# Performance work log

Hardware: AMD Instinct MI355X
Metric: run time of the kernel (lower is better)

## Reference

```python
import jax, jax.numpy as jnp
import numpy as np

D_MODEL = 1024
D_INNER = 2048
N_EXPERTS = 8
TOP_K = 2
INIT_STD = 0.02


def setup_inputs() -> dict:
    key = jax.random.key(0)
    ks = jax.random.split(key, 6)
    B, S = 2, 2048
    x = jax.random.normal(ks[0], (B, S, D_MODEL), dtype=jnp.float32)
    router_w = jax.random.normal(ks[1], (N_EXPERTS, D_MODEL), dtype=jnp.float32) * (INIT_STD * 0.1)
    router_b = jnp.zeros((N_EXPERTS,), dtype=jnp.float32)
    gate_w = jax.random.normal(ks[2], (N_EXPERTS, D_MODEL, D_INNER), dtype=jnp.float32) * INIT_STD
    up_w = jax.random.normal(ks[3], (N_EXPERTS, D_MODEL, D_INNER), dtype=jnp.float32) * INIT_STD
    down_w = jax.random.normal(ks[4], (N_EXPERTS, D_INNER, D_MODEL), dtype=jnp.float32) * INIT_STD
    return {"x": x, "router_w": router_w, "router_b": router_b,
            "gate_w": gate_w, "up_w": up_w, "down_w": down_w}


def reference(x, router_w, router_b, gate_w, up_w, down_w):
    # Router: softmax over experts, top-k, renormalize top-k probs.
    logits = jnp.einsum('bsd,ed->bse', x, router_w) + router_b          # [B,S,E]
    probs = jax.nn.softmax(logits, axis=-1)
    top_p, top_i = jax.lax.top_k(probs, TOP_K)                           # [B,S,K]
    top_p = top_p / jnp.sum(top_p, axis=-1, keepdims=True)
    # Per-expert combine weight: c[b,s,e] = sum_k top_p[b,s,k] * [top_i[b,s,k]==e]
    onehot = jax.nn.one_hot(top_i, N_EXPERTS, dtype=x.dtype)             # [B,S,K,E]
    combine = jnp.einsum('bsk,bske->bse', top_p, onehot)                 # [B,S,E]
    # SwiGLU FFN for every expert (dense form of the masked dispatch),
    # zeroed/weighted by combine coefficients.
    g = jnp.einsum('bsd,edf->ebsf', x, gate_w)                           # [E,B,S,F]
    u = jnp.einsum('bsd,edf->ebsf', x, up_w)
    h = jax.nn.silu(g) * u
    y = jnp.einsum('ebsf,efd->ebsd', h, down_w)                          # [E,B,S,D]
    out = jnp.einsum('ebsd,bse->bsd', y, combine)
    return out
```

## Files before the change

kernel.cpp:

```cpp
#include <hip/hip_runtime.h>
#include <hip/hip_bf16.h>
#include <stdint.h>

#define D_MODEL 1024
#define D_INNER 2048
#define NEXP 8
#define TOPK 2
#define T256 40
#define T128 72

typedef float f32x4 __attribute__((ext_vector_type(4)));
typedef short bf16x8 __attribute__((ext_vector_type(8)));

#define MEMFENCE asm volatile("" ::: "memory")
#define SB __builtin_amdgcn_sched_barrier(0)
#define LGKM0 asm volatile("s_waitcnt lgkmcnt(0)" ::: "memory")
#define VM0 asm volatile("s_waitcnt vmcnt(0)" ::: "memory")
#define VM4 asm volatile("s_waitcnt vmcnt(4)" ::: "memory")
#define BAR __builtin_amdgcn_s_barrier()
#define SW2(r) (((r) >> 1) & 3)

__device__ __forceinline__ unsigned short f2b(float f) {
    union { float f; uint32_t u; } v; v.f = f;
    uint32_t u = v.u;
    return (unsigned short)((u + 0x7fffu + ((u >> 16) & 1u)) >> 16);
}

__device__ __forceinline__ void gl_lds16(const void* g, void* l) {
    __builtin_amdgcn_global_load_lds((const __attribute__((address_space(1))) void*)g,
                                     (__attribute__((address_space(3))) void*)l, 16, 0, 0);
}

__global__ __launch_bounds__(256) void tcast3_kernel(
    const float* __restrict__ gw, const float* __restrict__ uw, const float* __restrict__ dw,
    unsigned short* __restrict__ gT, unsigned short* __restrict__ uT, unsigned short* __restrict__ dT)
{
    __shared__ unsigned short S[64][68];
    int which = blockIdx.z >> 3;
    int e = blockIdx.z & 7;
    const float* in; unsigned short* out; int K, N;
    if (which == 0)      { in = gw; out = gT; K = D_MODEL; N = D_INNER; }
    else if (which == 1) { in = uw; out = uT; K = D_MODEL; N = D_INNER; }
    else                 { in = dw; out = dT; K = D_INNER; N = D_MODEL; }
    int n0 = blockIdx.x * 64, k0 = blockIdx.y * 64;
    if (n0 >= N || k0 >= K) return;
    const float* ib = in + (size_t)e * K * N;
    unsigned short* ob = out + (size_t)e * N * K;
    int tid = threadIdx.x;
    int kk = tid >> 4, nn4 = (tid & 15) * 4;
#pragma unroll
    for (int j = 0; j < 4; j++) {
        int k = kk + 16 * j;
        float4 v = *(const float4*)&ib[(size_t)(k0 + k) * N + n0 + nn4];
        ushort4 s; s.x = f2b(v.x); s.y = f2b(v.y); s.z = f2b(v.z); s.w = f2b(v.w);
        *(ushort4*)&S[k][nn4] = s;
    }
    __syncthreads();
    int nn = tid >> 4, kk4 = (tid & 15) * 4;
#pragma unroll
    for (int j = 0; j < 4; j++) {
        int n = nn + 16 * j;
        ushort4 s;
        s.x = S[kk4 + 0][n]; s.y = S[kk4 + 1][n];
        s.z = S[kk4 + 2][n]; s.w = S[kk4 + 3][n];
        *(ushort4*)&ob[(size_t)(n0 + n) * K + k0 + kk4] = s;
    }
}

__global__ __launch_bounds__(64) void router_kernel(
    const float* __restrict__ x, const float* __restrict__ rw,
    const float* __restrict__ rb, unsigned short* __restrict__ xb,
    int* __restrict__ top_i, float* __restrict__ top_w, int T)
{
    int t = blockIdx.x;
    if (t >= T) return;
    int l = threadIdx.x;
    float xv[16];
#pragma unroll
    for (int i = 0; i < 16; i++) xv[i] = x[(size_t)t * D_MODEL + l + 64 * i];
#pragma unroll
    for (int i = 0; i < 16; i++) xb[(size_t)t * D_MODEL + l + 64 * i] = f2b(xv[i]);
    float logit[NEXP];
#pragma unroll
    for (int e = 0; e < NEXP; e++) {
        float acc = 0.f;
#pragma unroll
        for (int i = 0; i < 16; i++) acc += xv[i] * rw[e * D_MODEL + l + 64 * i];
#pragma unroll
        for (int s = 32; s > 0; s >>= 1) acc += __shfl_xor(acc, s, 64);
        logit[e] = acc + rb[e];
    }
    if (l == 0) {
        int i0 = 0; float m0 = logit[0];
#pragma unroll
        for (int e = 1; e < NEXP; e++) if (logit[e] > m0) { m0 = logit[e]; i0 = e; }
        int i1 = -1; float m1 = -3.0e38f;
#pragma unroll
        for (int e = 0; e < NEXP; e++) {
            if (e == i0) continue;
            if (logit[e] > m1) { m1 = logit[e]; i1 = e; }
        }
        float w0 = 1.f / (1.f + expf(m1 - m0));
        top_i[t * 2 + 0] = i0; top_i[t * 2 + 1] = i1;
        top_w[t * 2 + 0] = w0; top_w[t * 2 + 1] = 1.f - w0;
    }
}

__global__ __launch_bounds__(256) void bucket_kernel(
    const int* __restrict__ top_i, const float* __restrict__ top_w,
    int* __restrict__ meta, int* __restrict__ tok_of_slot,
    float* __restrict__ w_of_slot, int T)
{
    __shared__ int cnt[256][NEXP];
    __shared__ int pre[256][NEXP];
    __shared__ int tot[NEXP];
    __shared__ int off[NEXP + 1];
    int tid = threadIdx.x;
    int per = (T + 255) / 256;
    int t0 = tid * per;
    for (int e = 0; e < NEXP; e++) cnt[tid][e] = 0;
    for (int t = t0; t < t0 + per && t < T; t++)
        for (int k = 0; k < TOPK; k++) cnt[tid][top_i[t * 2 + k]]++;
    __syncthreads();
    if (tid < NEXP) {
        int run = 0;
        for (int i = 0; i < 256; i++) { pre[i][tid] = run; run += cnt[i][tid]; }
        tot[tid] = run;
    }
    __syncthreads();
    if (tid == 0) {
        off[0] = 0;
        for (int e = 0; e < NEXP; e++) off[e + 1] = off[e] + tot[e];
        for (int e = 0; e <= NEXP; e++) meta[e] = off[e];
        int nt = 0;
        for (int e = 0; e < NEXP; e++)
            for (int r = off[e]; r < off[e + 1]; r += 256)
                meta[16 + nt++] = (e << 16) | r;
        meta[11] = nt;
        for (; nt < T256; nt++) meta[16 + nt] = -1;
        nt = 0;
        for (int e = 0; e < NEXP; e++)
            for (int r = off[e]; r < off[e + 1]; r += 128)
                meta[64 + nt++] = (e << 16) | r;
        meta[12] = nt;
        for (; nt < T128; nt++) meta[64 + nt] = -1;
    }
    __syncthreads();
    int lc[NEXP];
#pragma unroll
    for (int e = 0; e < NEXP; e++) lc[e] = 0;
    for (int t = t0; t < t0 + per && t < T; t++) {
        for (int k = 0; k < TOPK; k++) {
            int e = top_i[t * 2 + k];
            int slot = off[e] + pre[tid][e] + lc[e]++;
            tok_of_slot[slot] = t;
            w_of_slot[slot] = top_w[t * 2 + k];
        }
    }
}

__global__ __launch_bounds__(256, 3) void moe_gate_up(
    const unsigned short* __restrict__ xb, const unsigned short* __restrict__ wgT,
    const unsigned short* __restrict__ wuT, const int* __restrict__ meta,
    const int* __restrict__ tok_of_slot, unsigned short* __restrict__ H)
{
    extern __shared__ __align__(16) unsigned short lds[];

    int lin = blockIdx.x;
    int strip = (lin & 7) * 4 + ((lin >> 3) & 3);
    int tix = lin >> 5;
    int packed = meta[64 + tix];
    if (packed < 0) return;
    int e = packed >> 16, row0 = packed & 0xffff;
    int Mloc = min(128, meta[e + 1] - row0);
    int f0 = strip * 64;

    int tid = threadIdx.x, wv = tid >> 6, lane = tid & 63;
    int lrow = lane & 15, kgrp = lane >> 4;
    int sel = wv & 1, wm = wv >> 1;
    int co = 8 * (kgrp ^ SW2(lrow));

    const unsigned short* sA[2];
    int dA[2];
#pragma unroll
    for (int j = 0; j < 2; j++) {
        int idx = j * 256 + tid;
        int r = idx >> 2, c = idx & 3;
        int slot = row0 + ((r < Mloc) ? r : 0);
        sA[j] = xb + (size_t)tok_of_slot[slot] * D_MODEL + 8 * (c ^ SW2(r));
        dA[j] = idx * 8;
    }
    const unsigned short *sG, *sU;
    {
        int r = tid >> 2, c = tid & 3;
        size_t wb = (size_t)e * D_MODEL * D_INNER + (size_t)(f0 + r) * D_MODEL + 8 * (c ^ SW2(r));
        sG = wgT + wb; sU = wuT + wb;
    }

    int aoff[4], boff[4];
#pragma unroll
    for (int i = 0; i < 4; i++) aoff[i] = (wm * 64 + i * 16 + lrow) * 32 + co;
    int bb = sel ? 6144 : 4096;
#pragma unroll
    for (int i = 0; i < 4; i++) boff[i] = bb + (i * 16 + lrow) * 32 + co;

    f32x4 acc[4][4];
#pragma unroll
    for (int i = 0; i < 4; i++)
#pragma unroll
        for (int j = 0; j < 4; j++) acc[i][j] = (f32x4){0.f, 0.f, 0.f, 0.f};

    auto stage = [&](int u) {
        int kk = u * 32;
        unsigned short* b = lds + (u % 3) * 8192;
        gl_lds16(sA[0] + kk, b + dA[0]);
        gl_lds16(sA[1] + kk, b + dA[1]);
        gl_lds16(sG + kk, b + 4096 + tid * 8);
        gl_lds16(sU + kk, b + 6144 + tid * 8);
    };

    bf16x8 a[4], bfr[4];
    auto load_frags = [&](int u) {
        const unsigned short* b = lds + (u % 3) * 8192;
#pragma unroll
        for (int i = 0; i < 4; i++) a[i] = *(const bf16x8*)(b + aoff[i]);
#pragma unroll
        for (int i = 0; i < 4; i++) bfr[i] = *(const bf16x8*)(b + boff[i]);
    };

    const int NT = D_MODEL / 32;
    stage(0); stage(1);
    MEMFENCE;
    VM4;
    BAR; MEMFENCE;
    load_frags(0);

    for (int t = 0; t < NT; ++t) {
        if (t + 2 < NT) stage(t + 2);
        SB;
        __builtin_amdgcn_s_setprio(1);
#pragma unroll
        for (int i = 0; i < 4; i++)
#pragma unroll
            for (int j = 0; j < 4; j++)
                acc[i][j] = __builtin_amdgcn_mfma_f32_16x16x32_bf16(a[i], bfr[j], acc[i][j], 0, 0, 0);
        __builtin_amdgcn_s_setprio(0);
        SB;
        LGKM0;
        if (t + 2 < NT) { VM4; } else { VM0; }
        BAR; MEMFENCE;
        if (t + 1 < NT) load_frags(t + 1);
    }

    __syncthreads();
    float* ex = (float*)lds;
    if (sel == 1) {
        float* dst = ex + wm * 4160;
#pragma unroll
        for (int i = 0; i < 4; i++)
#pragma unroll
            for (int j = 0; j < 4; j++)
#pragma unroll
                for (int r = 0; r < 4; r++)
                    dst[(i * 16 + kgrp * 4 + r) * 65 + j * 16 + lrow] = acc[i][j][r];
    }
    __syncthreads();
    if (sel == 0) {
        const float* src = ex + wm * 4160;
#pragma unroll
        for (int i = 0; i < 4; i++)
#pragma unroll
            for (int j = 0; j < 4; j++)
#pragma unroll
                for (int r = 0; r < 4; r++) {
                    int row = i * 16 + kgrp * 4 + r;
                    int m = wm * 64 + row;
                    if (m < Mloc) {
                        float g = acc[i][j][r];
                        float u = src[row * 65 + j * 16 + lrow];
                        float h = g / (1.f + __expf(-g)) * u;
                        H[(size_t)(row0 + m) * D_INNER + f0 + j * 16 + lrow] = f2b(h);
                    }
                }
    }
}

__global__ __launch_bounds__(256, 3) void moe_down(
    const unsigned short* __restrict__ H, const unsigned short* __restrict__ wdT,
    const int* __restrict__ meta, const int* __restrict__ tok_of_slot,
    const float* __restrict__ w_of_slot, float* __restrict__ out, int S2)
{
    extern __shared__ __align__(16) unsigned short lds[];
    __shared__ int toks[128];
    __shared__ float wts[128];

    int lin = blockIdx.x;
    int d0 = (lin & 7) * 128;
    int tix = lin >> 3;
    int packed = meta[64 + tix];
    if (packed < 0) return;
    int e = packed >> 16, row0 = packed & 0xffff;
    int Mloc = min(128, meta[e + 1] - row0);

    int tid = threadIdx.x, wv = tid >> 6, lane = tid & 63;
    int lrow = lane & 15, kgrp = lane >> 4;
    int wn = wv & 1, wm = wv >> 1;
    int co = 8 * (kgrp ^ SW2(lrow));

    if (tid < 128) {
        bool v = tid < Mloc;
        toks[tid] = v ? tok_of_slot[row0 + tid] : 0;
        wts[tid] = v ? w_of_slot[row0 + tid] : 0.f;
    }

    const unsigned short* sA[2];
    const unsigned short* sB[2];
    int dA[2];
#pragma unroll
    for (int j = 0; j < 2; j++) {
        int idx = j * 256 + tid;
        int r = idx >> 2, c = idx & 3;
        int slot = min(row0 + r, S2 - 1);
        sA[j] = H + (size_t)slot * D_INNER + 8 * (c ^ SW2(r));
        sB[j] = wdT + (size_t)e * D_INNER * D_MODEL + (size_t)(d0 + r) * D_INNER + 8 * (c ^ SW2(r));
        dA[j] = idx * 8;
    }

    int aoff[4], boff[4];
#pragma unroll
    for (int i = 0; i < 4; i++) aoff[i] = (wm * 64 + i * 16 + lrow) * 32 + co;
#pragma unroll
    for (int i = 0; i < 4; i++) boff[i] = 4096 + (wn * 64 + i * 16 + lrow) * 32 + co;

    f32x4 acc[4][4];
#pragma unroll
    for (int i = 0; i < 4; i++)
#pragma unroll
        for (int j = 0; j < 4; j++) acc[i][j] = (f32x4){0.f, 0.f, 0.f, 0.f};

    auto stage = [&](int u) {
        int kk = u * 32;
        unsigned short* b = lds + (u % 3) * 8192;
        gl_lds16(sA[0] + kk, b + dA[0]);
        gl_lds16(sA[1] + kk, b + dA[1]);
        gl_lds16(sB[0] + kk, b + 4096 + dA[0]);
        gl_lds16(sB[1] + kk, b + 4096 + dA[1]);
    };

    bf16x8 a[4], bfr[4];
    auto load_frags = [&](int u) {
        const unsigned short* b = lds + (u % 3) * 8192;
#pragma unroll
        for (int i = 0; i < 4; i++) a[i] = *(const bf16x8*)(b + aoff[i]);
#pragma unroll
        for (int i = 0; i < 4; i++) bfr[i] = *(const bf16x8*)(b + boff[i]);
    };

    const int NT = D_INNER / 32;
    stage(0); stage(1);
    MEMFENCE;
    VM4;
    BAR; MEMFENCE;
    load_frags(0);

    for (int t = 0; t < NT; ++t) {
        if (t + 2 < NT) stage(t + 2);
        SB;
        __builtin_amdgcn_s_setprio(1);
#pragma unroll
        for (int i = 0; i < 4; i++)
#pragma unroll
            for (int j = 0; j < 4; j++)
                acc[i][j] = __builtin_amdgcn_mfma_f32_16x16x32_bf16(a[i], bfr[j], acc[i][j], 0, 0, 0);
        __builtin_amdgcn_s_setprio(0);
        SB;
        LGKM0;
        if (t + 2 < NT) { VM4; } else { VM0; }
        BAR; MEMFENCE;
        if (t + 1 < NT) load_frags(t + 1);
    }

#pragma unroll
    for (int i = 0; i < 4; i++)
#pragma unroll
        for (int j = 0; j < 4; j++)
#pragma unroll
            for (int r = 0; r < 4; r++) {
                int m = wm * 64 + i * 16 + kgrp * 4 + r;
                if (m < Mloc) {
                    int n = d0 + wn * 64 + j * 16 + lrow;
                    atomicAdd(&out[(size_t)toks[m] * D_MODEL + n], wts[m] * acc[i][j][r]);
                }
            }
}

extern "C" void kernel_launch(void* const* d_in, const int* in_sizes, int n_in,
                              void* d_out, int out_size, void* d_ws, size_t ws_size,
                              hipStream_t stream) {
    const float* x  = (const float*)d_in[0];
    const float* rw = (const float*)d_in[1];
    const float* rb = (const float*)d_in[2];
    const float* gw = (const float*)d_in[3];
    const float* uw = (const float*)d_in[4];
    const float* dw = (const float*)d_in[5];
    float* out = (float*)d_out;

    int T = in_sizes[0] / D_MODEL;
    int S2 = 2 * T;

    char* ws = (char*)d_ws;
    size_t cur = 0;
    auto take = [&](size_t bytes) { char* p = ws + cur; cur = (cur + bytes + 255) & ~(size_t)255; return p; };
    int*   top_i = (int*)take((size_t)S2 * 4);
    float* top_w = (float*)take((size_t)S2 * 4);
    int*   meta  = (int*)take(1024);
    int*   tos   = (int*)take((size_t)S2 * 4);
    float* wos   = (float*)take((size_t)S2 * 4);
    unsigned short* xb  = (unsigned short*)take((size_t)T * D_MODEL * 2);
    unsigned short* wgT = (unsigned short*)take((size_t)NEXP * D_MODEL * D_INNER * 2);
    unsigned short* wuT = (unsigned short*)take((size_t)NEXP * D_MODEL * D_INNER * 2);
    unsigned short* wdT = (unsigned short*)take((size_t)NEXP * D_MODEL * D_INNER * 2);
    unsigned short* H   = (unsigned short*)take((size_t)S2 * D_INNER * 2);

    static const int RING_LDS = 3 * 8192 * 2;
    hipFuncSetAttribute((const void*)moe_gate_up,
                        hipFuncAttributeMaxDynamicSharedMemorySize, RING_LDS);
    hipFuncSetAttribute((const void*)moe_down,
                        hipFuncAttributeMaxDynamicSharedMemorySize, RING_LDS);

    hipMemsetAsync(d_out, 0, (size_t)out_size * sizeof(float), stream);

    tcast3_kernel<<<dim3(32, 32, 24), 256, 0, stream>>>(gw, uw, dw, wgT, wuT, wdT);
    router_kernel<<<T, 64, 0, stream>>>(x, rw, rb, xb, top_i, top_w, T);
    bucket_kernel<<<1, 256, 0, stream>>>(top_i, top_w, meta, tos, wos, T);

    moe_gate_up<<<T128 * 32, 256, RING_LDS, stream>>>(xb, wgT, wuT, meta, tos, H);
    moe_down<<<T128 * 8, 256, RING_LDS, stream>>>(H, wdT, meta, tos, wos, out, S2);
}
```

Measured before the change: 272.1 us.

## Enlarge MoE GEMM tiles to 512 threads with K=64 stages and split-K down

Both expert GEMMs move to 512-thread blocks with 64-wide K stages in a larger triple-buffered LDS ring, using an XOR swizzle over 8 chunks. Gate/up now covers 256-row token tiles via the T256 tile list, and down uses 256-column tiles with a two-way split-K that accumulates through atomics. Fragment loads and prefetch are interleaved with four MFMA quadrants per stage to overlap LDS reads with compute. The aim is more operand reuse and fewer weight reloads per token. In exchange it adds extra barriers per iteration, raises LDS per block, and doubles atomic traffic in the down projection.

New measurement: 315.4 us. 15.9% more time.

```diff
diff --git a/kernel.cpp b/kernel.cpp
--- a/kernel.cpp
+++ b/kernel.cpp
@@ -16,9 +16,17 @@
 #define SB __builtin_amdgcn_sched_barrier(0)
 #define LGKM0 asm volatile("s_waitcnt lgkmcnt(0)" ::: "memory")
 #define VM0 asm volatile("s_waitcnt vmcnt(0)" ::: "memory")
-#define VM4 asm volatile("s_waitcnt vmcnt(4)" ::: "memory")
+#define VM6 asm volatile("s_waitcnt vmcnt(6)" ::: "memory")
 #define BAR __builtin_amdgcn_s_barrier()
-#define SW2(r) (((r) >> 1) & 3)
+
+#define Q8(I0, J0, AF, BF)                                                        \
+  _Pragma("unroll") for (int i_ = 0; i_ < 2; i_++)                                \
+    _Pragma("unroll") for (int j_ = 0; j_ < 2; j_++) {                            \
+      acc[(I0) + i_][(J0) + j_] = __builtin_amdgcn_mfma_f32_16x16x32_bf16(        \
+          AF[2 * i_], BF[2 * j_], acc[(I0) + i_][(J0) + j_], 0, 0, 0);            \
+      acc[(I0) + i_][(J0) + j_] = __builtin_amdgcn_mfma_f32_16x16x32_bf16(        \
+          AF[2 * i_ + 1], BF[2 * j_ + 1], acc[(I0) + i_][(J0) + j_], 0, 0, 0);    \
+    }
 
 __device__ __forceinline__ unsigned short f2b(float f) {
     union { float f; uint32_t u; } v; v.f = f;
@@ -159,7 +167,7 @@
     }
 }
 
-__global__ __launch_bounds__(256, 3) void moe_gate_up(
+__global__ __launch_bounds__(512, 2) void moe_gate_up(
     const unsigned short* __restrict__ xb, const unsigned short* __restrict__ wgT,
     const unsigned short* __restrict__ wuT, const int* __restrict__ meta,
     const int* __restrict__ tok_of_slot, unsigned short* __restrict__ H)
@@ -169,40 +177,39 @@
     int lin = blockIdx.x;
     int strip = (lin & 7) * 4 + ((lin >> 3) & 3);
     int tix = lin >> 5;
-    int packed = meta[64 + tix];
+    int packed = meta[16 + tix];
     if (packed < 0) return;
     int e = packed >> 16, row0 = packed & 0xffff;
-    int Mloc = min(128, meta[e + 1] - row0);
+    int Mloc = min(256, meta[e + 1] - row0);
     int f0 = strip * 64;
 
     int tid = threadIdx.x, wv = tid >> 6, lane = tid & 63;
-    int lrow = lane & 15, kgrp = lane >> 4;
-    int sel = wv & 1, wm = wv >> 1;
-    int co = 8 * (kgrp ^ SW2(lrow));
-
-    const unsigned short* sA[2];
-    int dA[2];
-#pragma unroll
-    for (int j = 0; j < 2; j++) {
-        int idx = j * 256 + tid;
-        int r = idx >> 2, c = idx & 3;
+    int lrow = lane & 15, kgrp = lane >> 4, sw = lrow & 7;
+    int mh = wv >> 1, sel = wv & 1;
+    int co0 = 8 * (kgrp ^ sw);
+    int co1 = 8 * ((4 + kgrp) ^ sw);
+
+    int srow = tid >> 3, schk = tid & 7;
+    const unsigned short* sA[4];
+#pragma unroll
+    for (int j = 0; j < 4; j++) {
+        int r = j * 64 + srow;
         int slot = row0 + ((r < Mloc) ? r : 0);
-        sA[j] = xb + (size_t)tok_of_slot[slot] * D_MODEL + 8 * (c ^ SW2(r));
-        dA[j] = idx * 8;
+        sA[j] = xb + (size_t)tok_of_slot[slot] * D_MODEL + 8 * (schk ^ (r & 7));
     }
     const unsigned short *sG, *sU;
     {
-        int r = tid >> 2, c = tid & 3;
-        size_t wb = (size_t)e * D_MODEL * D_INNER + (size_t)(f0 + r) * D_MODEL + 8 * (c ^ SW2(r));
+        size_t wb = (size_t)e * D_MODEL * D_INNER + (size_t)(f0 + srow) * D_MODEL + 8 * (schk ^ (srow & 7));
         sG = wgT + wb; sU = wuT + wb;
     }
+    int dst = tid * 8;
 
     int aoff[4], boff[4];
 #pragma unroll
-    for (int i = 0; i < 4; i++) aoff[i] = (wm * 64 + i * 16 + lrow) * 32 + co;
-    int bb = sel ? 6144 : 4096;
-#pragma unroll
-    for (int i = 0; i < 4; i++) boff[i] = bb + (i * 16 + lrow) * 32 + co;
+    for (int i = 0; i < 4; i++) aoff[i] = (mh * 64 + i * 16 + lrow) * 64;
+    int bb = 16384 + sel * 4096;
+#pragma unroll
+    for (int i = 0; i < 4; i++) boff[i] = bb + (i * 16 + lrow) * 64;
 
     f32x4 acc[4][4];
 #pragma unroll
@@ -210,63 +217,81 @@
 #pragma unroll
         for (int j = 0; j < 4; j++) acc[i][j] = (f32x4){0.f, 0.f, 0.f, 0.f};
 
-    auto stage = [&](int u) {
-        int kk = u * 32;
-        unsigned short* b = lds + (u % 3) * 8192;
-        gl_lds16(sA[0] + kk, b + dA[0]);
-        gl_lds16(sA[1] + kk, b + dA[1]);
-        gl_lds16(sG + kk, b + 4096 + tid * 8);
-        gl_lds16(sU + kk, b + 6144 + tid * 8);
-    };
-
-    bf16x8 a[4], bfr[4];
-    auto load_frags = [&](int u) {
-        const unsigned short* b = lds + (u % 3) * 8192;
-#pragma unroll
-        for (int i = 0; i < 4; i++) a[i] = *(const bf16x8*)(b + aoff[i]);
-#pragma unroll
-        for (int i = 0; i < 4; i++) bfr[i] = *(const bf16x8*)(b + boff[i]);
-    };
-
-    const int NT = D_MODEL / 32;
-    stage(0); stage(1);
-    MEMFENCE;
-    VM4;
-    BAR; MEMFENCE;
-    load_frags(0);
+    auto stageA01 = [&](int u) {
+        int kk = u * 64; unsigned short* b = lds + (u % 3) * 24576;
+        gl_lds16(sA[0] + kk, b + dst);
+        gl_lds16(sA[1] + kk, b + 4096 + dst);
+    };
+    auto stageA23 = [&](int u) {
+        int kk = u * 64; unsigned short* b = lds + (u % 3) * 24576;
+        gl_lds16(sA[2] + kk, b + 8192 + dst);
+        gl_lds16(sA[3] + kk, b + 12288 + dst);
+    };
+    auto stageGU = [&](int u) {
+        int kk = u * 64; unsigned short* b = lds + (u % 3) * 24576;
+        gl_lds16(sG + kk, b + 16384 + dst);
+        gl_lds16(sU + kk, b + 20480 + dst);
+    };
+
+    bf16x8 A0[4], A1[4], B0[4], B1[4];
+
+    const int NT = D_MODEL / 64;
+    stageA01(0); stageA23(0); stageGU(0);
+    stageA01(1); stageA23(1); stageGU(1);
+    MEMFENCE; VM6; BAR; MEMFENCE;
 
     for (int t = 0; t < NT; ++t) {
-        if (t + 2 < NT) stage(t + 2);
+        const unsigned short* b = lds + (t % 3) * 24576;
+        bool pf = (t + 2) < NT;
+        A0[0] = *(const bf16x8*)(b + aoff[0] + co0);
+        A0[1] = *(const bf16x8*)(b + aoff[0] + co1);
+        A0[2] = *(const bf16x8*)(b + aoff[1] + co0);
+        A0[3] = *(const bf16x8*)(b + aoff[1] + co1);
+        B0[0] = *(const bf16x8*)(b + boff[0] + co0);
+        B0[1] = *(const bf16x8*)(b + boff[0] + co1);
+        B0[2] = *(const bf16x8*)(b + boff[1] + co0);
+        B0[3] = *(const bf16x8*)(b + boff[1] + co1);
+        if (pf) stageA01(t + 2);
+        SB; BAR; LGKM0; SB;
+        __builtin_amdgcn_s_setprio(1); Q8(0, 0, A0, B0); __builtin_amdgcn_s_setprio(0);
+        SB; BAR;
+        B1[0] = *(const bf16x8*)(b + boff[2] + co0);
+        B1[1] = *(const bf16x8*)(b + boff[2] + co1);
+        B1[2] = *(const bf16x8*)(b + boff[3] + co0);
+        B1[3] = *(const bf16x8*)(b + boff[3] + co1);
+        if (pf) stageA23(t + 2);
+        SB; BAR; LGKM0; SB;
+        __builtin_amdgcn_s_setprio(1); Q8(0, 2, A0, B1); __builtin_amdgcn_s_setprio(0);
+        SB; BAR;
+        A1[0] = *(const bf16x8*)(b + aoff[2] + co0);
+        A1[1] = *(const bf16x8*)(b + aoff[2] + co1);
+        A1[2] = *(const bf16x8*)(b + aoff[3] + co0);
+        A1[3] = *(const bf16x8*)(b + aoff[3] + co1);
+        if (pf) stageGU(t + 2);
+        SB; BAR; LGKM0; SB;
+        __builtin_amdgcn_s_setprio(1); Q8(2, 0, A1, B0); __builtin_amdgcn_s_setprio(0);
+        SB; BAR;
+        __builtin_amdgcn_s_setprio(1); Q8(2, 2, A1, B1); __builtin_amdgcn_s_setprio(0);
         SB;
-        __builtin_amdgcn_s_setprio(1);
-#pragma unroll
-        for (int i = 0; i < 4; i++)
-#pragma unroll
-            for (int j = 0; j < 4; j++)
-                acc[i][j] = __builtin_amdgcn_mfma_f32_16x16x32_bf16(a[i], bfr[j], acc[i][j], 0, 0, 0);
-        __builtin_amdgcn_s_setprio(0);
-        SB;
-        LGKM0;
-        if (t + 2 < NT) { VM4; } else { VM0; }
+        if (pf) { VM6; } else { VM0; }
         BAR; MEMFENCE;
-        if (t + 1 < NT) load_frags(t + 1);
     }
 
     __syncthreads();
     float* ex = (float*)lds;
     if (sel == 1) {
-        float* dst = ex + wm * 4160;
+        float* d = ex + mh * 4160;
 #pragma unroll
         for (int i = 0; i < 4; i++)
 #pragma unroll
             for (int j = 0; j < 4; j++)
 #pragma unroll
                 for (int r = 0; r < 4; r++)
-                    dst[(i * 16 + kgrp * 4 + r) * 65 + j * 16 + lrow] = acc[i][j][r];
+                    d[(i * 16 + kgrp * 4 + r) * 65 + j * 16 + lrow] = acc[i][j][r];
     }
     __syncthreads();
     if (sel == 0) {
-        const float* src = ex + wm * 4160;
+        const float* s = ex + mh * 4160;
 #pragma unroll
         for (int i = 0; i < 4; i++)
 #pragma unroll
@@ -274,10 +299,10 @@
 #pragma unroll
                 for (int r = 0; r < 4; r++) {
                     int row = i * 16 + kgrp * 4 + r;
-                    int m = wm * 64 + row;
+                    int m = mh * 64 + row;
                     if (m < Mloc) {
                         float g = acc[i][j][r];
-                        float u = src[row * 65 + j * 16 + lrow];
+                        float u = s[row * 65 + j * 16 + lrow];
                         float h = g / (1.f + __expf(-g)) * u;
                         H[(size_t)(row0 + m) * D_INNER + f0 + j * 16 + lrow] = f2b(h);
                     }
@@ -285,7 +310,7 @@
     }
 }
 
-__global__ __launch_bounds__(256, 3) void moe_down(
+__global__ __launch_bounds__(512, 2) void moe_down(
     const unsigned short* __restrict__ H, const unsigned short* __restrict__ wdT,
     const int* __restrict__ meta, const int* __restrict__ tok_of_slot,
     const float* __restrict__ w_of_slot, float* __restrict__ out, int S2)
@@ -295,17 +320,21 @@
     __shared__ float wts[128];
 
     int lin = blockIdx.x;
-    int d0 = (lin & 7) * 128;
+    int dstrip = lin & 3;
+    int kq = (lin >> 2) & 1;
     int tix = lin >> 3;
     int packed = meta[64 + tix];
     if (packed < 0) return;
     int e = packed >> 16, row0 = packed & 0xffff;
     int Mloc = min(128, meta[e + 1] - row0);
+    int d0 = dstrip * 256;
+    int kb = kq * 1024;
 
     int tid = threadIdx.x, wv = tid >> 6, lane = tid & 63;
-    int lrow = lane & 15, kgrp = lane >> 4;
-    int wn = wv & 1, wm = wv >> 1;
-    int co = 8 * (kgrp ^ SW2(lrow));
+    int lrow = lane & 15, kgrp = lane >> 4, sw = lrow & 7;
+    int mh = wv >> 2, nh = wv & 3;
+    int co0 = 8 * (kgrp ^ sw);
+    int co1 = 8 * ((4 + kgrp) ^ sw);
 
     if (tid < 128) {
         bool v = tid < Mloc;
@@ -313,24 +342,27 @@
         wts[tid] = v ? w_of_slot[row0 + tid] : 0.f;
     }
 
+    int srow = tid >> 3, schk = tid & 7;
     const unsigned short* sA[2];
-    const unsigned short* sB[2];
-    int dA[2];
 #pragma unroll
     for (int j = 0; j < 2; j++) {
-        int idx = j * 256 + tid;
-        int r = idx >> 2, c = idx & 3;
+        int r = j * 64 + srow;
         int slot = min(row0 + r, S2 - 1);
-        sA[j] = H + (size_t)slot * D_INNER + 8 * (c ^ SW2(r));
-        sB[j] = wdT + (size_t)e * D_INNER * D_MODEL + (size_t)(d0 + r) * D_INNER + 8 * (c ^ SW2(r));
-        dA[j] = idx * 8;
-    }
+        sA[j] = H + (size_t)slot * D_INNER + kb + 8 * (schk ^ (r & 7));
+    }
+    const unsigned short* sB[4];
+#pragma unroll
+    for (int j = 0; j < 4; j++) {
+        int r = j * 64 + srow;
+        sB[j] = wdT + (size_t)e * D_INNER * D_MODEL + (size_t)(d0 + r) * D_INNER + kb + 8 * (schk ^ (r & 7));
+    }
+    int dst = tid * 8;
 
     int aoff[4], boff[4];
 #pragma unroll
-    for (int i = 0; i < 4; i++) aoff[i] = (wm * 64 + i * 16 + lrow) * 32 + co;
-#pragma unroll
-    for (int i = 0; i < 4; i++) boff[i] = 4096 + (wn * 64 + i * 16 + lrow) * 32 + co;
+    for (int i = 0; i < 4; i++) aoff[i] = (mh * 64 + i * 16 + lrow) * 64;
+#pragma unroll
+    for (int i = 0; i < 4; i++) boff[i] = 8192 + (nh * 64 + i * 16 + lrow) * 64;
 
     f32x4 acc[4][4];
 #pragma unroll
@@ -338,46 +370,64 @@
 #pragma unroll
         for (int j = 0; j < 4; j++) acc[i][j] = (f32x4){0.f, 0.f, 0.f, 0.f};
 
-    auto stage = [&](int u) {
-        int kk = u * 32;
-        unsigned short* b = lds + (u % 3) * 8192;
-        gl_lds16(sA[0] + kk, b + dA[0]);
-        gl_lds16(sA[1] + kk, b + dA[1]);
-        gl_lds16(sB[0] + kk, b + 4096 + dA[0]);
-        gl_lds16(sB[1] + kk, b + 4096 + dA[1]);
-    };
-
-    bf16x8 a[4], bfr[4];
-    auto load_frags = [&](int u) {
-        const unsigned short* b = lds + (u % 3) * 8192;
-#pragma unroll
-        for (int i = 0; i < 4; i++) a[i] = *(const bf16x8*)(b + aoff[i]);
-#pragma unroll
-        for (int i = 0; i < 4; i++) bfr[i] = *(const bf16x8*)(b + boff[i]);
-    };
-
-    const int NT = D_INNER / 32;
-    stage(0); stage(1);
-    MEMFENCE;
-    VM4;
-    BAR; MEMFENCE;
-    load_frags(0);
+    auto stageA = [&](int u) {
+        int kk = u * 64; unsigned short* b = lds + (u % 3) * 24576;
+        gl_lds16(sA[0] + kk, b + dst);
+        gl_lds16(sA[1] + kk, b + 4096 + dst);
+    };
+    auto stageB01 = [&](int u) {
+        int kk = u * 64; unsigned short* b = lds + (u % 3) * 24576;
+        gl_lds16(sB[0] + kk, b + 8192 + dst);
+        gl_lds16(sB[1] + kk, b + 12288 + dst);
+    };
+    auto stageB23 = [&](int u) {
+        int kk = u * 64; unsigned short* b = lds + (u % 3) * 24576;
+        gl_lds16(sB[2] + kk, b + 16384 + dst);
+        gl_lds16(sB[3] + kk, b + 20480 + dst);
+    };
+
+    bf16x8 A0[4], A1[4], B0[4], B1[4];
+
+    const int NT = 1024 / 64;
+    stageA(0); stageB01(0); stageB23(0);
+    stageA(1); stageB01(1); stageB23(1);
+    MEMFENCE; VM6; BAR; MEMFENCE;
 
     for (int t = 0; t < NT; ++t) {
-        if (t + 2 < NT) stage(t + 2);
+        const unsigned short* b = lds + (t % 3) * 24576;
+        bool pf = (t + 2) < NT;
+        A0[0] = *(const bf16x8*)(b + aoff[0] + co0);
+        A0[1] = *(const bf16x8*)(b + aoff[0] + co1);
+        A0[2] = *(const bf16x8*)(b + aoff[1] + co0);
+        A0[3] = *(const bf16x8*)(b + aoff[1] + co1);
+        B0[0] = *(const bf16x8*)(b + boff[0] + co0);
+        B0[1] = *(const bf16x8*)(b + boff[0] + co1);
+        B0[2] = *(const bf16x8*)(b + boff[1] + co0);
+        B0[3] = *(const bf16x8*)(b + boff[1] + co1);
+        if (pf) stageA(t + 2);
+        SB; BAR; LGKM0; SB;
+        __builtin_amdgcn_s_setprio(1); Q8(0, 0, A0, B0); __builtin_amdgcn_s_setprio(0);
+        SB; BAR;
+        B1[0] = *(const bf16x8*)(b + boff[2] + co0);
+        B1[1] = *(const bf16x8*)(b + boff[2] + co1);
+        B1[2] = *(const bf16x8*)(b + boff[3] + co0);
+        B1[3] = *(const bf16x8*)(b + boff[3] + co1);
+        if (pf) stageB01(t + 2);
+        SB; BAR; LGKM0; SB;
+        __builtin_amdgcn_s_setprio(1); Q8(0, 2, A0, B1); __builtin_amdgcn_s_setprio(0);
+        SB; BAR;
+        A1[0] = *(const bf16x8*)(b + aoff[2] + co0);
+        A1[1] = *(const bf16x8*)(b + aoff[2] + co1);
+        A1[2] = *(const bf16x8*)(b + aoff[3] + co0);
+        A1[3] = *(const bf16x8*)(b + aoff[3] + co1);
+        if (pf) stageB23(t + 2);
+        SB; BAR; LGKM0; SB;
+        __builtin_amdgcn_s_setprio(1); Q8(2, 0, A1, B0); __builtin_amdgcn_s_setprio(0);
+        SB; BAR;
+        __builtin_amdgcn_s_setprio(1); Q8(2, 2, A1, B1); __builtin_amdgcn_s_setprio(0);
         SB;
-        __builtin_amdgcn_s_setprio(1);
-#pragma unroll
-        for (int i = 0; i < 4; i++)
-#pragma unroll
-            for (int j = 0; j < 4; j++)
-                acc[i][j] = __builtin_amdgcn_mfma_f32_16x16x32_bf16(a[i], bfr[j], acc[i][j], 0, 0, 0);
-        __builtin_amdgcn_s_setprio(0);
-        SB;
-        LGKM0;
-        if (t + 2 < NT) { VM4; } else { VM0; }
+        if (pf) { VM6; } else { VM0; }
         BAR; MEMFENCE;
-        if (t + 1 < NT) load_frags(t + 1);
     }
 
 #pragma unroll
@@ -386,9 +436,9 @@
         for (int j = 0; j < 4; j++)
 #pragma unroll
             for (int r = 0; r < 4; r++) {
-                int m = wm * 64 + i * 16 + kgrp * 4 + r;
+                int m = mh * 64 + i * 16 + kgrp * 4 + r;
                 if (m < Mloc) {
-                    int n = d0 + wn * 64 + j * 16 + lrow;
+                    int n = d0 + nh * 64 + j * 16 + lrow;
                     atomicAdd(&out[(size_t)toks[m] * D_MODEL + n], wts[m] * acc[i][j][r]);
                 }
             }
@@ -422,7 +472,7 @@
     unsigned short* wdT = (unsigned short*)take((size_t)NEXP * D_MODEL * D_INNER * 2);
     unsigned short* H   = (unsigned short*)take((size_t)S2 * D_INNER * 2);
 
-    static const int RING_LDS = 3 * 8192 * 2;
+    static const int RING_LDS = 3 * 24576 * 2;
     hipFuncSetAttribute((const void*)moe_gate_up,
                         hipFuncAttributeMaxDynamicSharedMemorySize, RING_LDS);
     hipFuncSetAttribute((const void*)moe_down,
@@ -434,6 +484,6 @@
     router_kernel<<<T, 64, 0, stream>>>(x, rw, rb, xb, top_i, top_w, T);
     bucket_kernel<<<1, 256, 0, stream>>>(top_i, top_w, meta, tos, wos, T);
 
-    moe_gate_up<<<T128 * 32, 256, RING_LDS, stream>>>(xb, wgT, wuT, meta, tos, H);
-    moe_down<<<T128 * 8, 256, RING_LDS, stream>>>(H, wdT, meta, tos, wos, out, S2);
-}
+    moe_gate_up<<<T256 * 32, 512, RING_LDS, stream>>>(xb, wgT, wuT, meta, tos, H);
+    moe_down<<<T128 * 8, 512, RING_LDS, stream>>>(H, wdT, meta, tos, wos, out, S2);
+}
```
